# Kernel optimization log

Hardware: AMD Instinct MI355X
Metric: run time of the kernel (lower is better)

Reference implementation:

```python
import jax, jax.numpy as jnp
import numpy as np

RADIUS = 11.0  # init kwarg
N, D = 8192, 64


def setup_inputs() -> dict:
    key = jax.random.key(0)
    kx, ka = jax.random.split(key)
    x = jax.random.normal(kx, (N, D), dtype=jnp.float32)
    adj = jax.random.randint(ka, (N, 16), 0, N, dtype=jnp.int32)  # unused by the layer
    return {"x": x, "adj": adj}


def reference(x, adj):
    # Pairwise Euclidean distances via Gram trick (same math as
    # sqrt(sum((x_i - x_j)^2)) but avoids materializing the [N, N, D] diff).
    sq = jnp.sum(x * x, axis=-1)                       # [N]
    d2 = sq[:, None] + sq[None, :] - 2.0 * (x @ x.T)    # [N, N]
    distances = jnp.sqrt(jnp.maximum(d2, 0.0))          # [N, N]
    mask = (distances <= RADIUS).astype(x.dtype)        # binary ball-query mask
    attention_scores = jax.nn.softmax(mask, axis=-1)    # softmax over 0/1 scores
    return attention_scores @ x                          # [N, D]
```

## Files before the change

kernel.cpp:

```cpp
#include <hip/hip_runtime.h>
#include <hip/hip_bf16.h>


#define NROWS 8192
#define NCHUNK 16
#define JPT 8

typedef __bf16 bf16x8 __attribute__((ext_vector_type(8)));
typedef float  f32x4  __attribute__((ext_vector_type(4)));
typedef unsigned int u32;
typedef u32 u32x4 __attribute__((ext_vector_type(4)));

#define MFMA16(A, B, C) __builtin_amdgcn_mfma_f32_16x16x32_bf16((A), (B), (C), 0, 0, 0)

#define GLOAD16(g, l)                                                     \
    __builtin_amdgcn_global_load_lds(                                     \
        (const __attribute__((address_space(1))) u32*)(g),                \
        (__attribute__((address_space(3))) u32*)(l), 16, 0, 0)

static __device__ __forceinline__ unsigned short bf16rn(float f) {
    unsigned u = __float_as_uint(f);
    unsigned r = u + 0x7FFFu + ((u >> 16) & 1u);
    return (unsigned short)(r >> 16);
}
static __device__ __forceinline__ float bf16tof(unsigned short h) {
    return __uint_as_float(((unsigned)h) << 16);
}

__global__ __launch_bounds__(256) void prep(const float* __restrict__ x,
                                            unsigned short* __restrict__ xhi,
                                            unsigned short* __restrict__ xlo,
                                            float* __restrict__ sq,
                                            float* __restrict__ S,
                                            float* __restrict__ cnt) {
    int t = blockIdx.x * 256 + threadIdx.x;
    int row = t >> 4, q = t & 15;
    const float4 v = *(const float4*)(x + ((size_t)row << 6) + (q << 2));
    float f0 = v.x, f1 = v.y, f2 = v.z, f3 = v.w;
    unsigned short h0 = bf16rn(f0), h1 = bf16rn(f1), h2 = bf16rn(f2), h3 = bf16rn(f3);
    unsigned short l0 = bf16rn(f0 - bf16tof(h0));
    unsigned short l1 = bf16rn(f1 - bf16tof(h1));
    unsigned short l2 = bf16rn(f2 - bf16tof(h2));
    unsigned short l3 = bf16rn(f3 - bf16tof(h3));
    uint2 ph, pl;
    ph.x = (u32)h0 | ((u32)h1 << 16);  ph.y = (u32)h2 | ((u32)h3 << 16);
    pl.x = (u32)l0 | ((u32)l1 << 16);  pl.y = (u32)l2 | ((u32)l3 << 16);
    *(uint2*)(xhi + ((size_t)row << 6) + (q << 2)) = ph;
    *(uint2*)(xlo + ((size_t)row << 6) + (q << 2)) = pl;
    float ss = f0 * f0;
    ss = fmaf(f1, f1, ss); ss = fmaf(f2, f2, ss); ss = fmaf(f3, f3, ss);
    ss += __shfl_xor(ss, 1); ss += __shfl_xor(ss, 2);
    ss += __shfl_xor(ss, 4); ss += __shfl_xor(ss, 8);
    if (q == 0) sq[row] = ss;
    f32x4 z = {0.f, 0.f, 0.f, 0.f};
    ((f32x4*)S)[t] = z;
    if (t < 2048) ((f32x4*)cnt)[t] = z;
}

static __device__ __forceinline__ int jslot(int j) {
    return (j & 32) | (((j >> 2) & 3) << 3) | (((j >> 4) & 1) << 2) | (j & 3);
}

__global__ __launch_bounds__(256, 2) void ballq_main(
        const unsigned short* __restrict__ xhi,
        const unsigned short* __restrict__ xlo,
        const float* __restrict__ sq,
        float* __restrict__ S, float* __restrict__ cnt,
        float* __restrict__ stotp) {
    __shared__ char sHI[2][8192];
    __shared__ char sLO[2][8192];
    __shared__ char sJT[2][8192];
    __shared__ float sqJ[2][64];
    __shared__ float stcol[64];

    const int tid = threadIdx.x;
    const int w = tid >> 6, l = tid & 63, l16 = l & 15, lg = l >> 4;
    const int itile = blockIdx.x & 31, chunk = blockIdx.x >> 5;
    const int i0 = (itile << 8) + w * 64;
    const int jt0 = chunk * JPT;

    const int srow = l >> 3;
    const int schunk = (l & 7) ^ srow;
    const size_t gsoff = ((size_t)srow << 6) + (schunk << 3);

    const int sj = (tid & 31) * 2;
    const int sd0 = (tid >> 5) * 8;
    const int sslot2 = jslot(sj) * 2;

    bf16x8 ihi[4][2], ilo[4][2];
    float sqi[4];
#pragma unroll
    for (int mt = 0; mt < 4; ++mt) {
        int ir = i0 + mt * 16 + l16;
#pragma unroll
        for (int ks = 0; ks < 2; ++ks) {
            size_t off = (size_t)ir * 64 + ks * 32 + lg * 8;
            ihi[mt][ks] = *(const bf16x8*)(xhi + off);
            ilo[mt][ks] = *(const bf16x8*)(xlo + off);
        }
        sqi[mt] = sq[ir];
    }

    if (chunk == 0) {
        if (tid < 64) stcol[tid] = 0.f;
        __syncthreads();
        float sv[2][8];
#pragma unroll
        for (int ks = 0; ks < 2; ++ks)
#pragma unroll
            for (int e = 0; e < 8; ++e) {
                float s = 0.f;
#pragma unroll
                for (int mt = 0; mt < 4; ++mt) {
                    const unsigned short* hp = (const unsigned short*)&ihi[mt][ks];
                    const unsigned short* lp = (const unsigned short*)&ilo[mt][ks];
                    s += bf16tof(hp[e]) + bf16tof(lp[e]);
                }
                s += __shfl_xor(s, 1); s += __shfl_xor(s, 2);
                s += __shfl_xor(s, 4); s += __shfl_xor(s, 8);
                sv[ks][e] = s;
            }
        if (l16 == 0) {
#pragma unroll
            for (int ks = 0; ks < 2; ++ks)
#pragma unroll
                for (int e = 0; e < 8; ++e)
                    atomicAdd(&stcol[ks * 32 + lg * 8 + e], sv[ks][e]);
        }
        __syncthreads();
        if (tid < 64) stotp[itile * 64 + tid] = stcol[tid];
    }

    f32x4 accS[4][4];
    u32 pcnt[4] = {0u, 0u, 0u, 0u};
#pragma unroll
    for (int a = 0; a < 4; ++a)
#pragma unroll
        for (int b = 0; b < 4; ++b) {
            accS[a][b][0] = 0.f; accS[a][b][1] = 0.f;
            accS[a][b][2] = 0.f; accS[a][b][3] = 0.f;
        }

    {
        int j0 = jt0 << 6;
        const unsigned short* gh = xhi + ((size_t)(j0 + w * 16) << 6) + gsoff;
        const unsigned short* gl = xlo + ((size_t)(j0 + w * 16) << 6) + gsoff;
        GLOAD16(gh,       &sHI[0][w * 16 * 128]);
        GLOAD16(gh + 512, &sHI[0][(w * 16 + 8) * 128]);
        GLOAD16(gl,       &sLO[0][w * 16 * 128]);
        GLOAD16(gl + 512, &sLO[0][(w * 16 + 8) * 128]);
        uint4 h0 = *(const uint4*)(xhi + (size_t)(j0 + sj) * 64 + sd0);
        uint4 h1 = *(const uint4*)(xhi + (size_t)(j0 + sj + 1) * 64 + sd0);
        float sqv = (tid < 64) ? sq[j0 + tid] : 0.f;
        const unsigned short* a0 = (const unsigned short*)&h0;
        const unsigned short* a1 = (const unsigned short*)&h1;
#pragma unroll
        for (int e = 0; e < 8; ++e) {
            u32 pv = (u32)a0[e] | ((u32)a1[e] << 16);
            *(u32*)(sJT[0] + (sd0 + e) * 128 + (sslot2 ^ (e << 4))) = pv;
        }
        if (tid < 64) sqJ[0][tid] = sqv;
    }
    __syncthreads();

    const int csw = (lg ^ (l16 & 7)) << 4;
    int buf = 0;
    for (int t = 0; t < JPT; ++t) {
        const bool more = (t + 1 < JPT);
        uint4 n0, n1; float nsq = 0.f;
        if (more) {
            int jn = (jt0 + t + 1) << 6;
            const unsigned short* gh = xhi + ((size_t)(jn + w * 16) << 6) + gsoff;
            const unsigned short* gl = xlo + ((size_t)(jn + w * 16) << 6) + gsoff;
            char* hb2 = sHI[buf ^ 1];
            char* lb2 = sLO[buf ^ 1];
            GLOAD16(gh,       hb2 + w * 16 * 128);
            GLOAD16(gh + 512, hb2 + (w * 16 + 8) * 128);
            GLOAD16(gl,       lb2 + w * 16 * 128);
            GLOAD16(gl + 512, lb2 + (w * 16 + 8) * 128);
            n0 = *(const uint4*)(xhi + (size_t)(jn + sj) * 64 + sd0);
            n1 = *(const uint4*)(xhi + (size_t)(jn + sj + 1) * 64 + sd0);
            if (tid < 64) nsq = sq[jn + tid];
        }

        const char* hb = sHI[buf];
        const char* lb = sLO[buf];
        u32 Fw[4][8];
#pragma unroll
        for (int nt = 0; nt < 4; ++nt) {
            const int ro = (nt * 16 + l16) * 128;
            bf16x8 jh[2], jl[2];
            jh[0] = *(const bf16x8*)(hb + ro + csw);
            jh[1] = *(const bf16x8*)(hb + ro + (csw ^ 64));
            jl[0] = *(const bf16x8*)(lb + ro + csw);
            jl[1] = *(const bf16x8*)(lb + ro + (csw ^ 64));
            f32x4 accD[4];
#pragma unroll
            for (int a = 0; a < 4; ++a) {
                accD[a][0] = 0.f; accD[a][1] = 0.f;
                accD[a][2] = 0.f; accD[a][3] = 0.f;
            }
#pragma unroll
            for (int ks = 0; ks < 2; ++ks)
#pragma unroll
                for (int mt = 0; mt < 4; ++mt) {
                    accD[mt] = MFMA16(jh[ks], ihi[mt][ks], accD[mt]);
                    accD[mt] = MFMA16(jh[ks], ilo[mt][ks], accD[mt]);
                    accD[mt] = MFMA16(jl[ks], ihi[mt][ks], accD[mt]);
                }
            const int kj = nt >> 1, s2 = (nt & 1) * 2;
            f32x4 sqr = *(const f32x4*)&sqJ[buf][nt * 16 + lg * 4];
#pragma unroll
            for (int mt = 0; mt < 4; ++mt) {
                float base = sqi[mt];
                bool in0 = fmaf(-2.f, accD[mt][0], base + sqr[0]) <= 121.f;
                bool in1 = fmaf(-2.f, accD[mt][1], base + sqr[1]) <= 121.f;
                bool in2 = fmaf(-2.f, accD[mt][2], base + sqr[2]) <= 121.f;
                bool in3 = fmaf(-2.f, accD[mt][3], base + sqr[3]) <= 121.f;
                Fw[mt][kj * 4 + s2 + 0] =
                    (in0 ? 0x3F80u : 0u) | (in1 ? 0x3F800000u : 0u);
                Fw[mt][kj * 4 + s2 + 1] =
                    (in2 ? 0x3F80u : 0u) | (in3 ? 0x3F800000u : 0u);
            }
        }
#pragma unroll
        for (int mt = 0; mt < 4; ++mt)
#pragma unroll
            for (int wd = 0; wd < 8; ++wd)
                pcnt[mt] += (u32)__builtin_popcount(Fw[mt][wd]);

#pragma unroll
        for (int kj = 0; kj < 2; ++kj) {
            bf16x8 m[4];
#pragma unroll
            for (int mt = 0; mt < 4; ++mt) {
                u32x4 fa = {Fw[mt][kj * 4 + 0], Fw[mt][kj * 4 + 1],
                            Fw[mt][kj * 4 + 2], Fw[mt][kj * 4 + 3]};
                m[mt] = __builtin_bit_cast(bf16x8, fa);
            }
#pragma unroll
            for (int ntd = 0; ntd < 4; ++ntd) {
                const char* bp = sJT[buf] + (ntd * 16 + l16) * 128 +
                                 ((kj * 64 + lg * 16) ^ ((l16 & 7) << 4));
                bf16x8 bT = *(const bf16x8*)bp;
#pragma unroll
                for (int mt = 0; mt < 4; ++mt)
                    accS[mt][ntd] = MFMA16(m[mt], bT, accS[mt][ntd]);
            }
        }

        if (more) {
            char* jb = sJT[buf ^ 1];
            const unsigned short* a0 = (const unsigned short*)&n0;
            const unsigned short* a1 = (const unsigned short*)&n1;
#pragma unroll
            for (int e = 0; e < 8; ++e) {
                u32 pv = (u32)a0[e] | ((u32)a1[e] << 16);
                *(u32*)(jb + (sd0 + e) * 128 + (sslot2 ^ (e << 4))) = pv;
            }
            if (tid < 64) sqJ[buf ^ 1][tid] = nsq;
        }
        __syncthreads();
        buf ^= 1;
    }

#pragma unroll
    for (int mt = 0; mt < 4; ++mt) {
        u32 v = pcnt[mt];
        v += __shfl_xor(v, 16);
        v += __shfl_xor(v, 32);
        if (lg == 0) atomicAdd(cnt + i0 + mt * 16 + l16, (float)(v / 7u));
    }
#pragma unroll
    for (int mt = 0; mt < 4; ++mt)
#pragma unroll
        for (int ntd = 0; ntd < 4; ++ntd)
#pragma unroll
            for (int r = 0; r < 4; ++r) {
                size_t idx = (size_t)(i0 + mt * 16 + lg * 4 + r) * 64 + ntd * 16 + l16;
                atomicAdd(S + idx, accS[mt][ntd][r]);
            }
}

__global__ __launch_bounds__(256) void ballq_combine(
        const float* __restrict__ S, const float* __restrict__ cnt,
        const float* __restrict__ stotp, float* __restrict__ out) {
    __shared__ float st[64];
    if (threadIdx.x < 64) {
        float s = 0.f;
#pragma unroll
        for (int g = 0; g < 32; ++g) s += stotp[g * 64 + threadIdx.x];
        st[threadIdx.x] = s;
    }
    __syncthreads();
    int t = blockIdx.x * 256 + threadIdx.x;
    int i = t >> 4, d0 = (t & 15) << 2;
    float c = cnt[i];
    f32x4 s = *(const f32x4*)(S + (size_t)i * 64 + d0);
    f32x4 stv = *(const f32x4*)&st[d0];
    const float K = 0.36787944117144233f;
    float den = 1.f / (c + K * (8192.f - c));
    f32x4 o;
#pragma unroll
    for (int k = 0; k < 4; ++k) o[k] = (s[k] + K * (stv[k] - s[k])) * den;
    *(f32x4*)(out + (size_t)i * 64 + d0) = o;
}

extern "C" void kernel_launch(void* const* d_in, const int* in_sizes, int n_in,
                              void* d_out, int out_size, void* d_ws, size_t ws_size,
                              hipStream_t stream) {
    (void)in_sizes; (void)n_in; (void)out_size; (void)ws_size;
    const float* x = (const float*)d_in[0];
    float* out = (float*)d_out;
    char* ws = (char*)d_ws;

    unsigned short* xhi = (unsigned short*)ws;
    unsigned short* xlo = (unsigned short*)(ws + (1u << 20));
    float* sq    = (float*)(ws + (2u << 20));
    float* S     = (float*)(ws + (2u << 20) + 32768);
    float* cnt   = (float*)(ws + (2u << 20) + 32768 + (1u << 21));
    float* stotp = (float*)(ws + (2u << 20) + 32768 + (1u << 21) + 32768);

    prep<<<512, 256, 0, stream>>>(x, xhi, xlo, sq, S, cnt);
    ballq_main<<<32 * NCHUNK, 256, 0, stream>>>(xhi, xlo, sq, S, cnt, stotp);
    ballq_combine<<<512, 256, 0, stream>>>(S, cnt, stotp, out);
}
```

Measured before the change: 120.4 us.

## Split main kernel i-tile across eight waves with 512-thread blocks

Each block now uses 512 threads (8 waves), and each wave owns 32 query rows instead of 64. That halves the per-wave MFMA accumulators and i-row fragments, and the cooperative LDS staging of j-tiles is reindexed so each wave loads a single row slice. The transpose staging loads shrink to 4 elements per thread, with the swizzle adjusted to match. The aim is more waves in flight and lower register pressure so latency is hidden better. In exchange, each LDS-staged j-tile is reused over fewer rows per wave, and barrier cost per block goes up.

```diff
diff --git a/kernel.cpp b/kernel.cpp
--- a/kernel.cpp
+++ b/kernel.cpp
@@ -61,7 +61,7 @@
     return (j & 32) | (((j >> 2) & 3) << 3) | (((j >> 4) & 1) << 2) | (j & 3);
 }
 
-__global__ __launch_bounds__(256, 2) void ballq_main(
+__global__ __launch_bounds__(512, 4) void ballq_main(
         const unsigned short* __restrict__ xhi,
         const unsigned short* __restrict__ xlo,
         const float* __restrict__ sq,
@@ -76,21 +76,22 @@
     const int tid = threadIdx.x;
     const int w = tid >> 6, l = tid & 63, l16 = l & 15, lg = l >> 4;
     const int itile = blockIdx.x & 31, chunk = blockIdx.x >> 5;
-    const int i0 = (itile << 8) + w * 64;
+    const int i0 = (itile << 8) + w * 32;
     const int jt0 = chunk * JPT;
 
-    const int srow = l >> 3;
-    const int schunk = (l & 7) ^ srow;
-    const size_t gsoff = ((size_t)srow << 6) + (schunk << 3);
+    const int srow = (w << 3) | (l >> 3);
+    const int schunk = (l & 7) ^ ((l >> 3) & 7);
+    const size_t gsoff = (size_t)srow * 64 + (schunk << 3);
+    const int ldsoff = w << 10;
 
     const int sj = (tid & 31) * 2;
-    const int sd0 = (tid >> 5) * 8;
+    const int sd0 = (tid >> 5) * 4;
     const int sslot2 = jslot(sj) * 2;
 
-    bf16x8 ihi[4][2], ilo[4][2];
-    float sqi[4];
-#pragma unroll
-    for (int mt = 0; mt < 4; ++mt) {
+    bf16x8 ihi[2][2], ilo[2][2];
+    float sqi[2];
+#pragma unroll
+    for (int mt = 0; mt < 2; ++mt) {
         int ir = i0 + mt * 16 + l16;
 #pragma unroll
         for (int ks = 0; ks < 2; ++ks) {
@@ -111,7 +112,7 @@
             for (int e = 0; e < 8; ++e) {
                 float s = 0.f;
 #pragma unroll
-                for (int mt = 0; mt < 4; ++mt) {
+                for (int mt = 0; mt < 2; ++mt) {
                     const unsigned short* hp = (const unsigned short*)&ihi[mt][ks];
                     const unsigned short* lp = (const unsigned short*)&ilo[mt][ks];
                     s += bf16tof(hp[e]) + bf16tof(lp[e]);
@@ -131,10 +132,10 @@
         if (tid < 64) stotp[itile * 64 + tid] = stcol[tid];
     }
 
-    f32x4 accS[4][4];
-    u32 pcnt[4] = {0u, 0u, 0u, 0u};
-#pragma unroll
-    for (int a = 0; a < 4; ++a)
+    f32x4 accS[2][4];
+    u32 pcnt[2] = {0u, 0u};
+#pragma unroll
+    for (int a = 0; a < 2; ++a)
 #pragma unroll
         for (int b = 0; b < 4; ++b) {
             accS[a][b][0] = 0.f; accS[a][b][1] = 0.f;
@@ -143,21 +144,17 @@
 
     {
         int j0 = jt0 << 6;
-        const unsigned short* gh = xhi + ((size_t)(j0 + w * 16) << 6) + gsoff;
-        const unsigned short* gl = xlo + ((size_t)(j0 + w * 16) << 6) + gsoff;
-        GLOAD16(gh,       &sHI[0][w * 16 * 128]);
-        GLOAD16(gh + 512, &sHI[0][(w * 16 + 8) * 128]);
-        GLOAD16(gl,       &sLO[0][w * 16 * 128]);
-        GLOAD16(gl + 512, &sLO[0][(w * 16 + 8) * 128]);
-        uint4 h0 = *(const uint4*)(xhi + (size_t)(j0 + sj) * 64 + sd0);
-        uint4 h1 = *(const uint4*)(xhi + (size_t)(j0 + sj + 1) * 64 + sd0);
+        GLOAD16(xhi + ((size_t)j0 << 6) + gsoff, &sHI[0][ldsoff]);
+        GLOAD16(xlo + ((size_t)j0 << 6) + gsoff, &sLO[0][ldsoff]);
+        uint2 h0 = *(const uint2*)(xhi + (size_t)(j0 + sj) * 64 + sd0);
+        uint2 h1 = *(const uint2*)(xhi + (size_t)(j0 + sj + 1) * 64 + sd0);
         float sqv = (tid < 64) ? sq[j0 + tid] : 0.f;
         const unsigned short* a0 = (const unsigned short*)&h0;
         const unsigned short* a1 = (const unsigned short*)&h1;
 #pragma unroll
-        for (int e = 0; e < 8; ++e) {
+        for (int e = 0; e < 4; ++e) {
             u32 pv = (u32)a0[e] | ((u32)a1[e] << 16);
-            *(u32*)(sJT[0] + (sd0 + e) * 128 + (sslot2 ^ (e << 4))) = pv;
+            *(u32*)(sJT[0] + (sd0 + e) * 128 + (sslot2 ^ (((sd0 + e) & 7) << 4))) = pv;
         }
         if (tid < 64) sqJ[0][tid] = sqv;
     }
@@ -167,25 +164,19 @@
     int buf = 0;
     for (int t = 0; t < JPT; ++t) {
         const bool more = (t + 1 < JPT);
-        uint4 n0, n1; float nsq = 0.f;
+        uint2 n0, n1; float nsq = 0.f;
         if (more) {
             int jn = (jt0 + t + 1) << 6;
-            const unsigned short* gh = xhi + ((size_t)(jn + w * 16) << 6) + gsoff;
-            const unsigned short* gl = xlo + ((size_t)(jn + w * 16) << 6) + gsoff;
-            char* hb2 = sHI[buf ^ 1];
-            char* lb2 = sLO[buf ^ 1];
-            GLOAD16(gh,       hb2 + w * 16 * 128);
-            GLOAD16(gh + 512, hb2 + (w * 16 + 8) * 128);
-            GLOAD16(gl,       lb2 + w * 16 * 128);
-            GLOAD16(gl + 512, lb2 + (w * 16 + 8) * 128);
-            n0 = *(const uint4*)(xhi + (size_t)(jn + sj) * 64 + sd0);
-            n1 = *(const uint4*)(xhi + (size_t)(jn + sj + 1) * 64 + sd0);
+            GLOAD16(xhi + ((size_t)jn << 6) + gsoff, &sHI[buf ^ 1][ldsoff]);
+            GLOAD16(xlo + ((size_t)jn << 6) + gsoff, &sLO[buf ^ 1][ldsoff]);
+            n0 = *(const uint2*)(xhi + (size_t)(jn + sj) * 64 + sd0);
+            n1 = *(const uint2*)(xhi + (size_t)(jn + sj + 1) * 64 + sd0);
             if (tid < 64) nsq = sq[jn + tid];
         }
 
         const char* hb = sHI[buf];
         const char* lb = sLO[buf];
-        u32 Fw[4][8];
+        u32 Fw[2][8];
 #pragma unroll
         for (int nt = 0; nt < 4; ++nt) {
             const int ro = (nt * 16 + l16) * 128;
@@ -194,16 +185,16 @@
             jh[1] = *(const bf16x8*)(hb + ro + (csw ^ 64));
             jl[0] = *(const bf16x8*)(lb + ro + csw);
             jl[1] = *(const bf16x8*)(lb + ro + (csw ^ 64));
-            f32x4 accD[4];
-#pragma unroll
-            for (int a = 0; a < 4; ++a) {
+            f32x4 accD[2];
+#pragma unroll
+            for (int a = 0; a < 2; ++a) {
                 accD[a][0] = 0.f; accD[a][1] = 0.f;
                 accD[a][2] = 0.f; accD[a][3] = 0.f;
             }
 #pragma unroll
             for (int ks = 0; ks < 2; ++ks)
 #pragma unroll
-                for (int mt = 0; mt < 4; ++mt) {
+                for (int mt = 0; mt < 2; ++mt) {
                     accD[mt] = MFMA16(jh[ks], ihi[mt][ks], accD[mt]);
                     accD[mt] = MFMA16(jh[ks], ilo[mt][ks], accD[mt]);
                     accD[mt] = MFMA16(jl[ks], ihi[mt][ks], accD[mt]);
@@ -211,7 +202,7 @@
             const int kj = nt >> 1, s2 = (nt & 1) * 2;
             f32x4 sqr = *(const f32x4*)&sqJ[buf][nt * 16 + lg * 4];
 #pragma unroll
-            for (int mt = 0; mt < 4; ++mt) {
+            for (int mt = 0; mt < 2; ++mt) {
                 float base = sqi[mt];
                 bool in0 = fmaf(-2.f, accD[mt][0], base + sqr[0]) <= 121.f;
                 bool in1 = fmaf(-2.f, accD[mt][1], base + sqr[1]) <= 121.f;
@@ -224,28 +215,26 @@
             }
         }
 #pragma unroll
-        for (int mt = 0; mt < 4; ++mt)
+        for (int mt = 0; mt < 2; ++mt)
 #pragma unroll
             for (int wd = 0; wd < 8; ++wd)
                 pcnt[mt] += (u32)__builtin_popcount(Fw[mt][wd]);
 
 #pragma unroll
         for (int kj = 0; kj < 2; ++kj) {
-            bf16x8 m[4];
-#pragma unroll
-            for (int mt = 0; mt < 4; ++mt) {
-                u32x4 fa = {Fw[mt][kj * 4 + 0], Fw[mt][kj * 4 + 1],
-                            Fw[mt][kj * 4 + 2], Fw[mt][kj * 4 + 3]};
-                m[mt] = __builtin_bit_cast(bf16x8, fa);
-            }
+            u32x4 fa0 = {Fw[0][kj * 4 + 0], Fw[0][kj * 4 + 1],
+                         Fw[0][kj * 4 + 2], Fw[0][kj * 4 + 3]};
+            u32x4 fa1 = {Fw[1][kj * 4 + 0], Fw[1][kj * 4 + 1],
+                         Fw[1][kj * 4 + 2], Fw[1][kj * 4 + 3]};
+            bf16x8 m0 = __builtin_bit_cast(bf16x8, fa0);
+            bf16x8 m1 = __builtin_bit_cast(bf16x8, fa1);
 #pragma unroll
             for (int ntd = 0; ntd < 4; ++ntd) {
                 const char* bp = sJT[buf] + (ntd * 16 + l16) * 128 +
                                  ((kj * 64 + lg * 16) ^ ((l16 & 7) << 4));
                 bf16x8 bT = *(const bf16x8*)bp;
-#pragma unroll
-                for (int mt = 0; mt < 4; ++mt)
-                    accS[mt][ntd] = MFMA16(m[mt], bT, accS[mt][ntd]);
+                accS[0][ntd] = MFMA16(m0, bT, accS[0][ntd]);
+                accS[1][ntd] = MFMA16(m1, bT, accS[1][ntd]);
             }
         }
 
@@ -254,9 +243,9 @@
             const unsigned short* a0 = (const unsigned short*)&n0;
             const unsigned short* a1 = (const unsigned short*)&n1;
 #pragma unroll
-            for (int e = 0; e < 8; ++e) {
+            for (int e = 0; e < 4; ++e) {
                 u32 pv = (u32)a0[e] | ((u32)a1[e] << 16);
-                *(u32*)(jb + (sd0 + e) * 128 + (sslot2 ^ (e << 4))) = pv;
+                *(u32*)(jb + (sd0 + e) * 128 + (sslot2 ^ (((sd0 + e) & 7) << 4))) = pv;
             }
             if (tid < 64) sqJ[buf ^ 1][tid] = nsq;
         }
@@ -265,14 +254,14 @@
     }
 
 #pragma unroll
-    for (int mt = 0; mt < 4; ++mt) {
+    for (int mt = 0; mt < 2; ++mt) {
         u32 v = pcnt[mt];
         v += __shfl_xor(v, 16);
         v += __shfl_xor(v, 32);
         if (lg == 0) atomicAdd(cnt + i0 + mt * 16 + l16, (float)(v / 7u));
     }
 #pragma unroll
-    for (int mt = 0; mt < 4; ++mt)
+    for (int mt = 0; mt < 2; ++mt)
 #pragma unroll
         for (int ntd = 0; ntd < 4; ++ntd)
 #pragma unroll
@@ -322,6 +311,6 @@
     float* stotp = (float*)(ws + (2u << 20) + 32768 + (1u << 21) + 32768);
 
     prep<<<512, 256, 0, stream>>>(x, xhi, xlo, sq, S, cnt);
-    ballq_main<<<32 * NCHUNK, 256, 0, stream>>>(xhi, xlo, sq, S, cnt, stotp);
+    ballq_main<<<32 * NCHUNK, 512, 0, stream>>>(xhi, xlo, sq, S, cnt, stotp);
     ballq_combine<<<512, 256, 0, stream>>>(S, cnt, stotp, out);
 }
```

Result: slower. 125.2 us (+4.0%).
